# Performance work log

Hardware: AMD Instinct MI355X
Metric: run time of the kernel (lower is better)

Reference implementation:

```python
import jax, jax.numpy as jnp
import numpy as np

N = 1536        # nodes in batch
E = 24576       # directed edges (avg in-degree 16)
H_DIM = 128     # hidden_dim
D = 1280        # input_dim (esm embedding size)
K_HOPS = 2
RATIO = 0.5     # node-drop pooling keep ratio
NEG = -1e9

def _leaky(v):
    return jnp.where(v > 0, v, 0.2 * v)

def setup_inputs():
    key = jax.random.key(0)
    ks = jax.random.split(key, 11)
    x = jax.random.normal(ks[0], (N, H_DIM), jnp.float32)
    x_orig = jax.random.normal(ks[1], (N, D), jnp.float32) * 0.1
    edge_index = jax.random.randint(ks[2], (2, E), 0, N, dtype=jnp.int32)
    batch = jnp.zeros((N,), jnp.int32)
    W1 = jax.random.normal(ks[3], (H_DIM, D), jnp.float32) / np.sqrt(H_DIM).astype(np.float32)
    a_src1 = jax.random.normal(ks[4], (D,), jnp.float32) / np.sqrt(D).astype(np.float32)
    a_dst1 = jax.random.normal(ks[5], (D,), jnp.float32) / np.sqrt(D).astype(np.float32)
    b1 = jnp.zeros((D,), jnp.float32)
    w2 = jax.random.normal(ks[6], (D,), jnp.float32) / np.sqrt(D).astype(np.float32)
    a_s2 = jax.random.normal(ks[7], (), jnp.float32)
    a_d2 = jax.random.normal(ks[8], (), jnp.float32)
    b2 = jnp.zeros((), jnp.float32)
    return {"x": x, "x_orig": x_orig, "edge_index": edge_index, "batch": batch,
            "W1": W1, "a_src1": a_src1, "a_dst1": a_dst1, "b1": b1,
            "w2": w2, "a_s2": a_s2, "a_d2": a_d2, "b2": b2}

def _forward(x, x_orig, edge_index, batch, W1, a_src1, a_dst1, b1, w2, a_s2, a_d2, b2):
    n = x.shape[0]
    src, tgt = edge_index[0], edge_index[1]
    sl = jnp.arange(n, dtype=src.dtype)
    src2 = jnp.concatenate([src, sl])   # PyG GATConv adds self-loops
    tgt2 = jnp.concatenate([tgt, sl])

    # ---- conv1: GATConv(hidden_dim -> input_dim, heads=1) on full graph ----
    h = x @ W1                                          # [N, D]
    e = _leaky((h @ a_src1)[src2] + (h @ a_dst1)[tgt2])  # [E+N]
    mx = jax.ops.segment_max(e, tgt2, num_segments=n)
    ex = jnp.exp(e - mx[tgt2])
    den = jax.ops.segment_sum(ex, tgt2, num_segments=n)
    alpha = ex / den[tgt2]
    x_gat = jax.ops.segment_sum(alpha[:, None] * h[src2], tgt2, num_segments=n) + b1

    # ---- batched k-hop ego masks (flow source->target, center included) ----
    A = jnp.zeros((n, n), jnp.float32).at[src, tgt].set(1.0)
    M = jnp.eye(n, dtype=jnp.float32)
    for _ in range(K_HOPS):
        M = jnp.minimum(M + M @ A.T, 1.0)
    Mb = M > 0                                          # [N_ego, N_node]

    # ---- pooling scorer GAT(D->1) on x_sub = x_gat[v] * x_orig[u] ----
    # h2[v,u] = sum_d x_gat[v,d] * x_orig[u,d] * w2[d]
    H2 = (x_gat * w2) @ x_orig.T                        # [N_ego, N_node]
    hs, ht = H2[:, src2], H2[:, tgt2]                   # [N_ego, E+N]
    valid = Mb[:, src2] & Mb[:, tgt2]
    e2 = jnp.where(valid, _leaky(a_s2 * hs + a_d2 * ht), NEG)

    def row(e_row, hs_row):  # attention softmax + aggregate within one ego
        m = jax.ops.segment_max(e_row, tgt2, num_segments=n)
        w = jnp.exp(e_row - m[tgt2])
        d = jax.ops.segment_sum(w, tgt2, num_segments=n)
        nu = jax.ops.segment_sum(w * hs_row, tgt2, num_segments=n)
        return nu / jnp.maximum(d, 1e-12)
    score = jax.vmap(row)(e2, hs) + b2                  # [N_ego, N_node]

    # ---- node-drop pooling: keep top ceil(RATIO*|ego|) nodes per ego ----
    size = jnp.sum(Mb, axis=1).astype(jnp.float32)
    k_keep = jnp.ceil(RATIO * size).astype(jnp.int32)
    score_m = jnp.where(Mb, score, NEG)
    order = jnp.argsort(-score_m, axis=1)
    rank = jnp.argsort(order, axis=1)
    keep = (rank < k_keep[:, None]) & Mb
    out = jnp.where(keep, jax.nn.sigmoid(score), 0.0)   # padded score matrix
    return out, keep

def reference(x, x_orig, edge_index, batch, W1, a_src1, a_dst1, b1, w2, a_s2, a_d2, b2):
    return _forward(x, x_orig, edge_index, batch, W1, a_src1, a_dst1, b1, w2, a_s2, a_d2, b2)
```

## Files before the change

### kernel.cpp

```cpp
#include <hip/hip_runtime.h>
#include <math.h>

#define N 1536
#define E 24576
#define HD 128
#define D 1280
#define NW 24
#define RT 16
#define KSP 4
#define KSL 320

#define NB_SPLIT 1920
#define NB_DEG   102
#define NB_H     480

typedef unsigned long long u64;
typedef unsigned short u16;
typedef unsigned int u32;
typedef __attribute__((ext_vector_type(8))) short bf16x8;
typedef __attribute__((ext_vector_type(4))) float f32x4;

#define GLDS(g, l) __builtin_amdgcn_global_load_lds( \
    (const __attribute__((address_space(1))) unsigned int*)(g), \
    (__attribute__((address_space(3))) unsigned int*)(l), 16, 0, 0)

__device__ __forceinline__ double lrelu(double v){ return v > 0.0 ? v : 0.2*v; }

__device__ __forceinline__ double fexp(double x){
    double n = __builtin_rint(x * 1.4426950408889634);
    double r = __builtin_fma(-n, 0.6931471805599453, x);
    r = __builtin_fma(-n, 2.3190468138462996e-17, r);
    double p = 2.505210838544172e-8;
    p = __builtin_fma(p, r, 2.755731922398589e-7);
    p = __builtin_fma(p, r, 2.7557319223985893e-6);
    p = __builtin_fma(p, r, 2.48015873015873e-5);
    p = __builtin_fma(p, r, 1.984126984126984e-4);
    p = __builtin_fma(p, r, 1.3888888888888889e-3);
    p = __builtin_fma(p, r, 8.333333333333333e-3);
    p = __builtin_fma(p, r, 4.1666666666666664e-2);
    p = __builtin_fma(p, r, 1.6666666666666666e-1);
    p = __builtin_fma(p, r, 0.5);
    p = __builtin_fma(p, r, 1.0);
    p = __builtin_fma(p, r, 1.0);
    long long ni = (long long)n;
    double s = __longlong_as_double((u64)(ni + 1023) << 52);
    return (x < -700.0) ? 0.0 : p * s;
}

__device__ __forceinline__ float fexpf_(float x){
    float n = __builtin_rintf(x * 1.44269504f);
    float r = __builtin_fmaf(-n, 0.693359375f, x);
    r = __builtin_fmaf(-n, -2.12194440e-4f, r);
    float p = 1.9841270e-4f;
    p = __builtin_fmaf(p, r, 1.3888889e-3f);
    p = __builtin_fmaf(p, r, 8.3333333e-3f);
    p = __builtin_fmaf(p, r, 4.1666667e-2f);
    p = __builtin_fmaf(p, r, 1.6666667e-1f);
    p = __builtin_fmaf(p, r, 0.5f);
    p = __builtin_fmaf(p, r, 1.0f);
    p = __builtin_fmaf(p, r, 1.0f);
    int ni = (int)n;
    float s = __uint_as_float((u32)(ni + 127) << 23);
    return p * s;
}

__device__ __forceinline__ void bsplit(float f, u16& h, u16& l){
    unsigned u = __float_as_uint(f);
    unsigned hr = (u + 0x7fffu + ((u>>16)&1u)) >> 16;
    h = (u16)hr;
    float hf = __uint_as_float(hr << 16);
    float r = f - hf;
    unsigned u2 = __float_as_uint(r);
    l = (u16)((u2 + 0x7fffu + ((u2>>16)&1u)) >> 16);
}

__global__ void k_prep(const float* __restrict__ xo, u16* __restrict__ Xhi, u16* __restrict__ Xlo,
                       const int* __restrict__ ei, u64* __restrict__ IN, int* __restrict__ deg,
                       const float* __restrict__ x, const float* __restrict__ W1,
                       float* __restrict__ h32){
    int bid = blockIdx.x, tid = threadIdx.x;
    if (bid < NB_SPLIT){
        int idx = (bid*256 + tid)*4;
        float4 v = *(const float4*)&xo[idx];
        ushort4 h, l;
        bsplit(v.x, h.x, l.x); bsplit(v.y, h.y, l.y);
        bsplit(v.z, h.z, l.z); bsplit(v.w, h.w, l.w);
        *(ushort4*)&Xhi[idx] = h;
        *(ushort4*)&Xlo[idx] = l;
    } else if (bid < NB_SPLIT + NB_DEG){
        int idx = (bid - NB_SPLIT)*256 + tid;
        if (idx < E){
            int s = ei[idx], t = ei[E+idx];
            atomicOr(&IN[(size_t)t*NW + (s>>6)], 1ULL << (s&63));
            atomicAdd(&deg[t], 1);
        } else if (idx < E+N){
            atomicAdd(&deg[idx-E], 1);
        }
    } else {
        int r = bid - (NB_SPLIT + NB_DEG);
        int rb = (r/5)*RT;
        int col = (r%5)*256 + tid;
        __shared__ float xL[RT*HD];
        for (int u=tid; u<RT*HD; u+=256) xL[u] = x[(size_t)rb*HD + u];
        __syncthreads();
        float acc[RT];
        #pragma unroll
        for (int rr=0; rr<RT; rr++) acc[rr] = 0.0f;
        const float* wp = &W1[col];
        #pragma unroll 4
        for (int k=0; k<HD; k++){
            float w = wp[(size_t)k*D];
            #pragma unroll
            for (int rr=0; rr<RT; rr++) acc[rr] = __builtin_fmaf(w, xL[rr*HD + k], acc[rr]);
        }
        #pragma unroll
        for (int rr=0; rr<RT; rr++) h32[(size_t)(rb+rr)*D + col] = acc[rr];
    }
}

__global__ void k_graph(const int* __restrict__ deg, int* __restrict__ coff, int* __restrict__ cursor,
                        const u64* __restrict__ IN, u64* __restrict__ Mb,
                        u16* __restrict__ cols, int* __restrict__ cnt){
    int tid = threadIdx.x;
    if (blockIdx.x == 0){
        __shared__ int ls[256];
        int v[6]; int s = 0;
        for (int u=0; u<6; u++){ v[u] = s; s += deg[tid*6+u]; }
        ls[tid] = s; __syncthreads();
        for (int d=1; d<256; d<<=1){
            int t2 = (tid>=d) ? ls[tid-d] : 0;
            __syncthreads();
            ls[tid] += t2;
            __syncthreads();
        }
        int base = (tid>0) ? ls[tid-1] : 0;
        for (int u=0; u<6; u++){
            int o = base + v[u];
            coff[tid*6+u] = o; cursor[tid*6+u] = o;
        }
        if (tid==255) coff[N] = ls[255];
        return;
    }
    int i = blockIdx.x - 1, ln = tid;
    __shared__ int scn[256];
    __shared__ u16 lst[N];
    u64 b = 0;
    if (ln < NW){
        b = IN[(size_t)i*NW + ln];
        if ((i>>6) == ln) b |= 1ULL << (i&63);
    }
    int pc = (ln < NW) ? __popcll(b) : 0;
    scn[ln] = pc; __syncthreads();
    for (int d=1; d<64; d<<=1){
        int v = (ln>=d) ? scn[ln-d] : 0;
        __syncthreads();
        scn[ln] += v;
        __syncthreads();
    }
    {
        int idx = scn[ln] - pc;
        u64 bb = b;
        while (bb){
            int k = __ffsll((unsigned long long)bb) - 1;
            bb &= bb - 1;
            lst[idx++] = (u16)(ln*64 + k);
        }
    }
    __syncthreads();
    int nn = scn[63];
    u64 R0 = b, R1 = 0, R2 = 0, R3 = 0;
    int u = 0;
    if (ln < NW){
        for (; u+3 < nn; u += 4){
            R0 |= IN[(size_t)lst[u  ]*NW + ln];
            R1 |= IN[(size_t)lst[u+1]*NW + ln];
            R2 |= IN[(size_t)lst[u+2]*NW + ln];
            R3 |= IN[(size_t)lst[u+3]*NW + ln];
        }
        for (; u < nn; u++) R0 |= IN[(size_t)lst[u]*NW + ln];
    }
    u64 R = (R0 | R1) | (R2 | R3);
    if (ln < NW) Mb[(size_t)i*NW + ln] = R;
    __syncthreads();
    pc = (ln < NW) ? __popcll(R) : 0;
    scn[ln] = pc; __syncthreads();
    for (int d=1; d<64; d<<=1){
        int v = (ln>=d) ? scn[ln-d] : 0;
        __syncthreads();
        scn[ln] += v;
        __syncthreads();
    }
    if (ln == 63) cnt[i] = scn[63];
    int idx = scn[ln] - pc;
    u64 bb = R;
    while (bb){
        int k = __ffsll((unsigned long long)bb) - 1;
        bb &= bb - 1;
        cols[(size_t)i*N + idx++] = (u16)(ln*64 + k);
    }
}

__global__ void k_fill_hv(const int* __restrict__ ei, int* __restrict__ cursor, u16* __restrict__ csr_src,
                          const float* __restrict__ h32, const float* __restrict__ as1,
                          const float* __restrict__ ad1, double* __restrict__ hs1,
                          double* __restrict__ hd1){
    int tid = threadIdx.x;
    if (blockIdx.x < NB_DEG){
        int idx = blockIdx.x*256 + tid;
        if (idx < E){
            int s = ei[idx], t = ei[E+idx];
            int p = atomicAdd(&cursor[t], 1);
            csr_src[p] = (u16)s;
        } else if (idx < E+N){
            int t = idx - E;
            int p = atomicAdd(&cursor[t], 1);
            csr_src[p] = (u16)t;
        }
        return;
    }
    int i = blockIdx.x - NB_DEG;
    __shared__ double ra[256], rb[256];
    double a = 0, b = 0;
    for (int d=tid; d<D; d+=256){
        double hv = (double)h32[(size_t)i*D + d];
        a += hv * (double)as1[d];
        b += hv * (double)ad1[d];
    }
    ra[tid] = a; rb[tid] = b; __syncthreads();
    for (int s=128; s>0; s>>=1){
        if (tid < s){ ra[tid] += ra[tid+s]; rb[tid] += rb[tid+s]; }
        __syncthreads();
    }
    if (tid == 0){ hs1[i] = ra[0]; hd1[i] = rb[0]; }
}

__global__ void k_gat(const int* __restrict__ coff, const u16* __restrict__ csr_src,
                      const double* __restrict__ hs1, const double* __restrict__ hd1,
                      const float* __restrict__ h32,
                      const float* __restrict__ b1, const float* __restrict__ w2,
                      u16* __restrict__ Ghi, u16* __restrict__ Glo){
    int t = blockIdx.x, tid = threadIdx.x;
    int o0 = coff[t], o1 = coff[t+1], dg = o1 - o0;
    __shared__ double red[256];
    __shared__ float als[256];
    __shared__ int ssrc[256];
    __shared__ double DD;
    double hdt = hd1[t];
    double dsum = 0.0;
    for (int j=tid; j<dg; j+=256){
        int s = csr_src[o0+j];
        double e = lrelu(hs1[s] + hdt);
        dsum += fexp(e);
    }
    red[tid] = dsum; __syncthreads();
    for (int step=128; step>0; step>>=1){
        if (tid < step) red[tid] += red[tid+step];
        __syncthreads();
    }
    if (tid == 0) DD = red[0];
    __syncthreads();
    double Dv = DD;
    float acc[5] = {0,0,0,0,0};
    for (int base=0; base<dg; base+=256){
        int j = base + tid;
        if (j < dg){
            int s = csr_src[o0+j];
            double e = lrelu(hs1[s] + hdt);
            als[tid] = (float)(fexp(e)/Dv); ssrc[tid] = s;
        }
        __syncthreads();
        int lim = min(256, dg-base);
        for (int u=0; u<lim; u+=2){
            float a0 = als[u];
            int s0 = ssrc[u];
            bool h1 = (u+1 < lim);
            float a1 = h1 ? als[u+1] : 0.0f;
            int s1 = h1 ? ssrc[u+1] : s0;
            const float* hp0 = &h32[(size_t)s0*D];
            const float* hp1 = &h32[(size_t)s1*D];
            #pragma unroll
            for (int q=0; q<5; q++)
                acc[q] = __builtin_fmaf(a1, hp1[tid + 256*q],
                         __builtin_fmaf(a0, hp0[tid + 256*q], acc[q]));
        }
        __syncthreads();
    }
    #pragma unroll
    for (int q=0; q<5; q++){
        int d = tid + 256*q;
        float g = (acc[q] + b1[d]) * w2[d];
        u16 gh, gl;
        bsplit(g, gh, gl);
        Ghi[(size_t)t*D + d] = gh;
        Glo[(size_t)t*D + d] = gl;
    }
}

__global__ __launch_bounds__(512, 4)
void k_h2mm(const u16* __restrict__ Ghi, const u16* __restrict__ Glo,
            const u16* __restrict__ Xhi, const u16* __restrict__ Xlo,
            float* __restrict__ Hp){
    __shared__ u16 As_hi[128*32], As_lo[128*32], Bs_hi[128*32], Bs_lo[128*32];
    int tid = threadIdx.x;
    int ks = blockIdx.x & (KSP-1);
    int tile = blockIdx.x >> 2;
    int bm = tile / 12, bn = tile % 12;
    int k0 = ks * KSL;
    int w = tid >> 6, L = tid & 63;
    int sr = w*16 + (L >> 2);
    int sc = (L & 3) * 8;
    size_t gA = (size_t)(bm*128 + sr)*D + k0 + sc;
    size_t gB = (size_t)(bn*128 + sr)*D + k0 + sc;
    int lw = w * 512;
    int l16 = L & 15, qd = L >> 4;
    int wm = (w & 1)*64, wn = (w >> 1)*32;
    f32x4 acc[4][2];
    #pragma unroll
    for (int a=0; a<4; a++)
        #pragma unroll
        for (int b=0; b<2; b++) acc[a][b] = (f32x4){0.f,0.f,0.f,0.f};

    for (int kb = 0; kb < KSL; kb += 32){
        __syncthreads();
        GLDS(Ghi + gA + kb, As_hi + lw);
        GLDS(Glo + gA + kb, As_lo + lw);
        GLDS(Xhi + gB + kb, Bs_hi + lw);
        GLDS(Xlo + gB + kb, Bs_lo + lw);
        __syncthreads();
        bf16x8 ahi[4], alo[4];
        #pragma unroll
        for (int tm=0; tm<4; tm++){
            ahi[tm] = *(const bf16x8*)&As_hi[(wm + tm*16 + l16)*32 + qd*8];
            alo[tm] = *(const bf16x8*)&As_lo[(wm + tm*16 + l16)*32 + qd*8];
        }
        #pragma unroll
        for (int tn=0; tn<2; tn++){
            bf16x8 bhf = *(const bf16x8*)&Bs_hi[(wn + tn*16 + l16)*32 + qd*8];
            bf16x8 blf = *(const bf16x8*)&Bs_lo[(wn + tn*16 + l16)*32 + qd*8];
            #pragma unroll
            for (int tm=0; tm<4; tm++){
                acc[tm][tn] = __builtin_amdgcn_mfma_f32_16x16x32_bf16(ahi[tm], bhf, acc[tm][tn], 0, 0, 0);
                acc[tm][tn] = __builtin_amdgcn_mfma_f32_16x16x32_bf16(alo[tm], bhf, acc[tm][tn], 0, 0, 0);
                acc[tm][tn] = __builtin_amdgcn_mfma_f32_16x16x32_bf16(ahi[tm], blf, acc[tm][tn], 0, 0, 0);
            }
        }
    }
    float* HO = Hp + (size_t)ks*N*N;
    #pragma unroll
    for (int tm=0; tm<4; tm++){
        int rbase = bm*128 + wm + tm*16 + qd*4;
        #pragma unroll
        for (int tn=0; tn<2; tn++){
            int cg = bn*128 + wn + tn*16 + l16;
            #pragma unroll
            for (int reg=0; reg<4; reg++)
                HO[(size_t)(rbase+reg)*N + cg] = acc[tm][tn][reg];
        }
    }
}

__global__ void k_score_rank(const float* __restrict__ Hp, const u64* __restrict__ Mb,
                             const u16* __restrict__ cols, const int* __restrict__ cnt,
                             const int* __restrict__ coff, const u16* __restrict__ csr_src,
                             const float* __restrict__ pas2, const float* __restrict__ pad2,
                             const float* __restrict__ pb2, float* __restrict__ out){
    int i = blockIdx.x, tid = threadIdx.x;
    __shared__ __align__(16) float HL[N];
    __shared__ u64 MbL[NW];
    __shared__ u16 clL[N];
    __shared__ u64 KL[N];
    __shared__ int hist[256];
    __shared__ u64 sPrefix;
    __shared__ int sKK;
    float* keepO = out + (size_t)N*N;
    {
        const float4* P0 = (const float4*)(Hp + (size_t)i*N);
        const float4* P1 = (const float4*)(Hp + (size_t)N*N   + (size_t)i*N);
        const float4* P2 = (const float4*)(Hp + (size_t)2*N*N + (size_t)i*N);
        const float4* P3 = (const float4*)(Hp + (size_t)3*N*N + (size_t)i*N);
        float4* H4 = (float4*)HL;
        for (int u=tid; u<N/4; u+=256){
            float4 a=P0[u], b=P1[u], c=P2[u], d=P3[u];
            float4 r;
            r.x = (a.x+b.x)+(c.x+d.x);
            r.y = (a.y+b.y)+(c.y+d.y);
            r.z = (a.z+b.z)+(c.z+d.z);
            r.w = (a.w+b.w)+(c.w+d.w);
            H4[u] = r;
        }
    }
    if (tid < NW) MbL[tid] = Mb[(size_t)i*NW + tid];
    __syncthreads();
    float as2 = pas2[0], ad2 = pad2[0];
    double b2 = (double)pb2[0];
    int c0 = cnt[i];
    c0 = min(max(c0, 0), N);
    for (int c=tid; c<c0; c+=256){
        int t = cols[(size_t)i*N + c];
        float ht = HL[t];
        float zd = ad2 * ht;
        int o0 = coff[t], o1 = coff[t+1];
        double den = 0.0, nu = 0.0;
        int p = o0;
        for (; p+7 < o1; p += 8){
            int s[8]; float h[8]; float wv[8];
            #pragma unroll
            for (int q=0; q<8; q++) s[q] = csr_src[p+q];
            #pragma unroll
            for (int q=0; q<8; q++) h[q] = HL[s[q]];
            #pragma unroll
            for (int q=0; q<8; q++){
                bool v = (MbL[s[q]>>6] >> (s[q]&63)) & 1ULL;
                float z = __builtin_fmaf(as2, h[q], zd);
                float e = z > 0.f ? z : 0.2f*z;
                e = fminf(fmaxf(e, -80.f), 80.f);
                wv[q] = v ? fexpf_(e) : 0.0f;
            }
            #pragma unroll
            for (int q=0; q<8; q++){
                den += (double)wv[q];
                nu  += (double)(wv[q]*h[q]);
            }
        }
        for (; p < o1; p++){
            int s = csr_src[p];
            bool v = (MbL[s>>6] >> (s&63)) & 1ULL;
            float hs = HL[s];
            float z = __builtin_fmaf(as2, hs, zd);
            float e = z > 0.0f ? z : 0.2f*z;
            e = fminf(fmaxf(e, -80.0f), 80.0f);
            float w = v ? fexpf_(e) : 0.0f;
            den += (double)w;
            nu  += (double)(w * hs);
        }
        float sf = (float)(nu / fmax(den, 1e-12) + b2);
        clL[c] = (u16)t;
        u32 kb = __float_as_uint(sf);
        kb = (kb & 0x80000000u) ? ~kb : (kb | 0x80000000u);
        KL[c] = ((u64)kb << 16) | (u32)(1535 - t);
    }
    __syncthreads();
    for (int d=tid; d<N; d+=256) HL[d] = 0.0f;
    int k = (c0 + 1) >> 1;
    if (tid == 0){ sPrefix = 0; sKK = k; }
    #pragma unroll 1
    for (int shift = 40; shift >= 0; shift -= 8){
        hist[tid] = 0;
        __syncthreads();
        u64 pref = sPrefix;
        int kkr = sKK;
        for (int c=tid; c<c0; c+=256){
            u64 key = KL[c];
            if ((key >> (shift+8)) == (pref >> (shift+8)))
                atomicAdd(&hist[(int)((key>>shift)&255)], 1);
        }
        __syncthreads();
        if (tid < 64){
            int Lx = tid;
            int b0 = hist[4*Lx], b1v = hist[4*Lx+1], b2v = hist[4*Lx+2], b3v = hist[4*Lx+3];
            int tot = ((b0 + b1v) + (b2v + b3v));
            int run = tot;
            #pragma unroll
            for (int d=1; d<64; d<<=1){
                int o = __shfl_down(run, d);
                if (Lx + d < 64) run += o;
            }
            int after = run - tot;
            int s3 = b3v + after, s2 = b2v + s3, s1 = b1v + s2, s0 = b0 + s1;
            int dg = -1, rem = 0;
            if (s0 >= kkr && s1 < kkr){ dg = 4*Lx;   rem = kkr - s1; }
            else if (s1 >= kkr && s2 < kkr){ dg = 4*Lx+1; rem = kkr - s2; }
            else if (s2 >= kkr && s3 < kkr){ dg = 4*Lx+2; rem = kkr - s3; }
            else if (s3 >= kkr && after < kkr){ dg = 4*Lx+3; rem = kkr - after; }
            if (dg >= 0){
                sPrefix = pref | ((u64)(u32)dg << shift);
                sKK = rem;
            }
        }
        __syncthreads();
    }
    u64 T = sPrefix;
    for (int p=tid; p<c0; p+=256){
        u64 Kp = KL[p];
        if (Kp >= T){
            u32 kb = (u32)(Kp >> 16);
            u32 orig = (kb & 0x80000000u) ? (kb & 0x7fffffffu) : ~kb;
            float sf = __uint_as_float(orig);
            HL[clL[p]] = 1.0f/(1.0f + fexpf_(fminf(fmaxf(-sf,-80.f),80.f)));
        }
    }
    __syncthreads();
    {
        const float4* H4 = (const float4*)HL;
        float4* O0 = (float4*)(out   + (size_t)i*N);
        float4* O1 = (float4*)(keepO + (size_t)i*N);
        for (int u=tid; u<N/4; u+=256){
            float4 s = H4[u];
            float4 kk;
            kk.x = (s.x > 0.0f) ? 1.0f : 0.0f;
            kk.y = (s.y > 0.0f) ? 1.0f : 0.0f;
            kk.z = (s.z > 0.0f) ? 1.0f : 0.0f;
            kk.w = (s.w > 0.0f) ? 1.0f : 0.0f;
            O0[u] = s;
            O1[u] = kk;
        }
    }
}

extern "C" void kernel_launch(void* const* d_in, const int* in_sizes, int n_in,
                              void* d_out, int out_size, void* d_ws, size_t ws_size,
                              hipStream_t stream){
    const float* x   = (const float*)d_in[0];
    const float* xo  = (const float*)d_in[1];
    const int*   ei  = (const int*)  d_in[2];
    const float* W1  = (const float*)d_in[4];
    const float* as1 = (const float*)d_in[5];
    const float* ad1 = (const float*)d_in[6];
    const float* b1  = (const float*)d_in[7];
    const float* w2  = (const float*)d_in[8];
    const float* as2 = (const float*)d_in[9];
    const float* ad2 = (const float*)d_in[10];
    const float* b2  = (const float*)d_in[11];
    float* out = (float*)d_out;

    char* w = (char*)d_ws;
    size_t o = 0;
    auto alloc = [&](size_t b)->char*{ char* r = w + o; o = (o + b + 255) & ~(size_t)255; return r; };

    float*  h32   = (float*) alloc((size_t)N*D*4);
    float*  Hp    = (float*) alloc((size_t)KSP*N*N*4);
    u16*    Ghi   = (u16*)   alloc((size_t)N*D*2);
    u16*    Glo   = (u16*)   alloc((size_t)N*D*2);
    u16*    Xhi   = (u16*)   alloc((size_t)N*D*2);
    u16*    Xlo   = (u16*)   alloc((size_t)N*D*2);
    u64*    IN    = (u64*)   alloc((size_t)N*NW*8);
    int*    deg   = (int*)   alloc((size_t)N*4);
    u64*    Mb    = (u64*)   alloc((size_t)N*NW*8);
    double* hs1   = (double*)alloc((size_t)N*8);
    double* hd1   = (double*)alloc((size_t)N*8);
    int*    coff  = (int*)   alloc((size_t)(N+1)*4);
    int*    cursor= (int*)   alloc((size_t)N*4);
    u16*    csr   = (u16*)   alloc((size_t)(E+N)*2);
    u16*    cols  = (u16*)   alloc((size_t)N*N*2);
    int*    cnt   = (int*)   alloc((size_t)N*4);

    hipMemsetAsync(IN, 0, (size_t)N*NW*8 + (size_t)N*4, stream);

    k_prep   <<<NB_SPLIT + NB_DEG + NB_H, 256, 0, stream>>>(xo, Xhi, Xlo, ei, IN, deg, x, W1, h32);
    k_graph  <<<N + 1, 256, 0, stream>>>(deg, coff, cursor, IN, Mb, cols, cnt);
    k_fill_hv<<<NB_DEG + N, 256, 0, stream>>>(ei, cursor, csr, h32, as1, ad1, hs1, hd1);
    k_gat    <<<N, 256, 0, stream>>>(coff, csr, hs1, hd1, h32, b1, w2, Ghi, Glo);
    k_h2mm   <<<144*KSP, 512, 0, stream>>>(Ghi, Glo, Xhi, Xlo, Hp);
    k_score_rank<<<N, 256, 0, stream>>>(Hp, Mb, cols, cnt, coff, csr, as2, ad2, b2, out);
}
```

Before: 202.8 us.

## Double-buffer LDS loads in split-K GEMM and halve the K-split count

The H2 GEMM kernel now double-buffers its global-to-LDS loads, issuing the next K-slice before computing on the current one and synchronising with vmcnt waits and raw barriers. The K-split factor drops from 4 to 2, which halves the partial-sum buffers written and read back by the score/rank kernel. The cost is twice the LDS per block (64 KB), which may reduce occupancy, and half as many blocks in the GEMM grid.

```diff
diff --git a/kernel.cpp b/kernel.cpp
--- a/kernel.cpp
+++ b/kernel.cpp
@@ -7,8 +7,8 @@
 #define D 1280
 #define NW 24
 #define RT 16
-#define KSP 4
-#define KSL 320
+#define KSP 2
+#define KSL 640
 
 #define NB_SPLIT 1920
 #define NB_DEG   102
@@ -300,10 +300,10 @@
 void k_h2mm(const u16* __restrict__ Ghi, const u16* __restrict__ Glo,
             const u16* __restrict__ Xhi, const u16* __restrict__ Xlo,
             float* __restrict__ Hp){
-    __shared__ u16 As_hi[128*32], As_lo[128*32], Bs_hi[128*32], Bs_lo[128*32];
+    __shared__ u16 S[2*4*4096];
     int tid = threadIdx.x;
     int ks = blockIdx.x & (KSP-1);
-    int tile = blockIdx.x >> 2;
+    int tile = blockIdx.x >> 1;
     int bm = tile / 12, bn = tile % 12;
     int k0 = ks * KSL;
     int w = tid >> 6, L = tid & 63;
@@ -320,23 +320,39 @@
         #pragma unroll
         for (int b=0; b<2; b++) acc[a][b] = (f32x4){0.f,0.f,0.f,0.f};
 
-    for (int kb = 0; kb < KSL; kb += 32){
-        __syncthreads();
-        GLDS(Ghi + gA + kb, As_hi + lw);
-        GLDS(Glo + gA + kb, As_lo + lw);
-        GLDS(Xhi + gB + kb, Bs_hi + lw);
-        GLDS(Xlo + gB + kb, Bs_lo + lw);
-        __syncthreads();
+    #define STAGE(B, KB) do{ \
+        GLDS(Ghi + gA + (KB), S + ((B)*4+0)*4096 + lw); \
+        GLDS(Glo + gA + (KB), S + ((B)*4+1)*4096 + lw); \
+        GLDS(Xhi + gB + (KB), S + ((B)*4+2)*4096 + lw); \
+        GLDS(Xlo + gB + (KB), S + ((B)*4+3)*4096 + lw); \
+    }while(0)
+
+    STAGE(0, 0);
+    const int NT = KSL/32;
+    #pragma unroll 1
+    for (int t = 0; t < NT; t++){
+        int cur = t & 1;
+        if (t+1 < NT){
+            STAGE(cur^1, (t+1)*32);
+            asm volatile("s_waitcnt vmcnt(4)" ::: "memory");
+        } else {
+            asm volatile("s_waitcnt vmcnt(0)" ::: "memory");
+        }
+        __builtin_amdgcn_s_barrier();
+        const u16* Ah = S + (cur*4+0)*4096;
+        const u16* Al = S + (cur*4+1)*4096;
+        const u16* Bh = S + (cur*4+2)*4096;
+        const u16* Bl = S + (cur*4+3)*4096;
         bf16x8 ahi[4], alo[4];
         #pragma unroll
         for (int tm=0; tm<4; tm++){
-            ahi[tm] = *(const bf16x8*)&As_hi[(wm + tm*16 + l16)*32 + qd*8];
-            alo[tm] = *(const bf16x8*)&As_lo[(wm + tm*16 + l16)*32 + qd*8];
+            ahi[tm] = *(const bf16x8*)&Ah[(wm + tm*16 + l16)*32 + qd*8];
+            alo[tm] = *(const bf16x8*)&Al[(wm + tm*16 + l16)*32 + qd*8];
         }
         #pragma unroll
         for (int tn=0; tn<2; tn++){
-            bf16x8 bhf = *(const bf16x8*)&Bs_hi[(wn + tn*16 + l16)*32 + qd*8];
-            bf16x8 blf = *(const bf16x8*)&Bs_lo[(wn + tn*16 + l16)*32 + qd*8];
+            bf16x8 bhf = *(const bf16x8*)&Bh[(wn + tn*16 + l16)*32 + qd*8];
+            bf16x8 blf = *(const bf16x8*)&Bl[(wn + tn*16 + l16)*32 + qd*8];
             #pragma unroll
             for (int tm=0; tm<4; tm++){
                 acc[tm][tn] = __builtin_amdgcn_mfma_f32_16x16x32_bf16(ahi[tm], bhf, acc[tm][tn], 0, 0, 0);
@@ -344,7 +360,9 @@
                 acc[tm][tn] = __builtin_amdgcn_mfma_f32_16x16x32_bf16(ahi[tm], blf, acc[tm][tn], 0, 0, 0);
             }
         }
-    }
+        __builtin_amdgcn_s_barrier();
+    }
+    #undef STAGE
     float* HO = Hp + (size_t)ks*N*N;
     #pragma unroll
     for (int tm=0; tm<4; tm++){
@@ -375,17 +393,12 @@
     float* keepO = out + (size_t)N*N;
     {
         const float4* P0 = (const float4*)(Hp + (size_t)i*N);
-        const float4* P1 = (const float4*)(Hp + (size_t)N*N   + (size_t)i*N);
-        const float4* P2 = (const float4*)(Hp + (size_t)2*N*N + (size_t)i*N);
-        const float4* P3 = (const float4*)(Hp + (size_t)3*N*N + (size_t)i*N);
+        const float4* P1 = (const float4*)(Hp + (size_t)N*N + (size_t)i*N);
         float4* H4 = (float4*)HL;
         for (int u=tid; u<N/4; u+=256){
-            float4 a=P0[u], b=P1[u], c=P2[u], d=P3[u];
+            float4 a=P0[u], b=P1[u];
             float4 r;
-            r.x = (a.x+b.x)+(c.x+d.x);
-            r.y = (a.y+b.y)+(c.y+d.y);
-            r.z = (a.z+b.z)+(c.z+d.z);
-            r.w = (a.w+b.w)+(c.w+d.w);
+            r.x = a.x+b.x; r.y = a.y+b.y; r.z = a.z+b.z; r.w = a.w+b.w;
             H4[u] = r;
         }
     }
```

Measured after the change: 202.7 us. About the same (-0.0%).
